# Optimization experiments

Hardware: AMD Instinct MI355X
Metric: run time of the kernel (lower is better)

Reference implementation:

```python
import jax, jax.numpy as jnp
import numpy as np

B, T, C = 4, 2048, 1024
QH = 4            # n_q_heads
D = C // QH       # per-head dim = 256
EPS = 1e-5


def setup_inputs() -> dict:
    key = jax.random.key(0)
    k1, k2, k3 = jax.random.split(key, 3)
    residual = jax.random.normal(k1, (B, T, C), dtype=jnp.float32)
    # scale weights ~ Xavier-ish so relu(score)^2 stays numerically sane
    w_fc = jax.random.normal(k2, (C, C), dtype=jnp.float32) * (1.0 / np.sqrt(C))
    w_proj = jax.random.normal(k3, (C, C), dtype=jnp.float32) * (1.0 / np.sqrt(C))
    ln_g = jnp.ones((C,), dtype=jnp.float32)
    ln_b = jnp.zeros((C,), dtype=jnp.float32)
    return {"residual": residual, "w_fc": w_fc, "w_proj": w_proj,
            "ln_g": ln_g, "ln_b": ln_b}


def _layernorm(x, g, b):
    mu = jnp.mean(x, axis=-1, keepdims=True)
    var = jnp.mean(jnp.square(x - mu), axis=-1, keepdims=True)
    return (x - mu) * jax.lax.rsqrt(var + EPS) * g + b


def reference(residual, w_fc, w_proj, ln_g, ln_b):
    Bx, Tx, Cx = residual.shape
    x = _layernorm(residual, ln_g, ln_b)
    # q: (B, QH, T, D)
    q = x.reshape(Bx, Tx, QH, D).transpose(0, 2, 1, 3)
    # keys: rows of w_fc chopped into 4C kv entries of dim D, shared across heads
    k = w_fc.reshape(-1, D)          # (S, D), S = 4C
    # values: columns of w_proj (i.e. w_proj^T rows) chopped the same way
    v = w_proj.T.reshape(-1, D)      # (S, D)
    scores = jnp.einsum('bhtd,sd->bhts', q, k)
    # softmax(log(relusq(score))) then *exp(lse) == plain relu(score)^2 weights
    p = jnp.square(jax.nn.relu(scores))
    out = jnp.einsum('bhts,sd->bhtd', p, v)
    out = out.transpose(0, 2, 1, 3).reshape(Bx, Tx, Cx)
    return residual + out
```

## Files before the change

### kernel.cpp

```cpp
#include <hip/hip_runtime.h>
#include <hip/hip_bf16.h>

typedef __attribute__((ext_vector_type(8))) short bf16x8;
typedef __attribute__((ext_vector_type(4))) float f32x4;

#define C_    1024
#define MROWS 32768
#define D_    256
#define S_TOT 4096
#define SCH   64
#define NCH   (S_TOT / SCH)

__device__ __forceinline__ unsigned short f2bf(float f) {
  union { float f; unsigned int u; } v; v.f = f;
  unsigned int u = v.u;
  u += 0x7fffu + ((u >> 16) & 1u);
  return (unsigned short)(u >> 16);
}

__device__ __forceinline__ void async16(const void* g, void* l) {
  __builtin_amdgcn_global_load_lds(
      (const __attribute__((address_space(1))) unsigned int*)g,
      (__attribute__((address_space(3))) unsigned int*)l, 16, 0, 0);
}

__global__ __launch_bounds__(256) void prep_all(
    const float* __restrict__ res, const float* __restrict__ g,
    const float* __restrict__ b, const float* __restrict__ wfc,
    const float* __restrict__ wproj,
    unsigned short* __restrict__ xq, unsigned short* __restrict__ kq,
    unsigned short* __restrict__ vq) {
  __shared__ unsigned short tile[8192];
  int bid = blockIdx.x;
  int tid = threadIdx.x;

  if (bid < 2048) {
    int wave = tid >> 6, lane = tid & 63;
    int row = bid * 4 + wave;
    const float* r = res + (size_t)row * C_;
    float4 x[4];
    float s = 0.f, s2 = 0.f;
    #pragma unroll
    for (int i = 0; i < 4; ++i) {
      x[i] = *(const float4*)(r + i * 256 + lane * 4);
      s  += x[i].x + x[i].y + x[i].z + x[i].w;
      s2 += x[i].x * x[i].x + x[i].y * x[i].y + x[i].z * x[i].z + x[i].w * x[i].w;
    }
    #pragma unroll
    for (int off = 32; off > 0; off >>= 1) {
      s  += __shfl_xor(s, off, 64);
      s2 += __shfl_xor(s2, off, 64);
    }
    float mu  = s * (1.0f / C_);
    float var = s2 * (1.0f / C_) - mu * mu;
    float rs  = rsqrtf(var + 1e-5f);
    #pragma unroll
    for (int i = 0; i < 4; ++i) {
      int c = i * 256 + lane * 4;
      float4 gg = *(const float4*)(g + c);
      float4 bb = *(const float4*)(b + c);
      unsigned short o[4];
      o[0] = f2bf((x[i].x - mu) * rs * gg.x + bb.x);
      o[1] = f2bf((x[i].y - mu) * rs * gg.y + bb.y);
      o[2] = f2bf((x[i].z - mu) * rs * gg.z + bb.z);
      o[3] = f2bf((x[i].w - mu) * rs * gg.w + bb.w);
      *(ushort4*)(xq + (size_t)row * C_ + c) = *(ushort4*)o;
    }
  } else if (bid < 2560) {
    int t = (bid - 2048) * 256 + tid;
    int lane = t & 63;
    int sn  = (t >> 6) & 1;
    int kc  = (t >> 7) & 7;
    int sc2 = t >> 10;
    int s = sc2 * 32 + sn * 16 + (lane & 15);
    int d = kc * 32 + (lane >> 4) * 8;
    const float* src = wfc + (size_t)s * D_ + d;
    float4 a = *(const float4*)src;
    float4 b2 = *(const float4*)(src + 4);
    unsigned short o[8] = { f2bf(a.x), f2bf(a.y), f2bf(a.z), f2bf(a.w),
                            f2bf(b2.x), f2bf(b2.y), f2bf(b2.z), f2bf(b2.w) };
    *(uint4*)(kq + (size_t)t * 8) = *(uint4*)o;
  } else {
    int bb = bid - 2560;
    int c0 = bb * 8;
    #pragma unroll
    for (int it = 0; it < 4; ++it) {
      int row = it * 256 + tid;
      const float* src = wproj + (size_t)row * C_ + c0;
      float4 a = *(const float4*)src;
      float4 b2 = *(const float4*)(src + 4);
      unsigned short* dst = &tile[row * 8];
      dst[0] = f2bf(a.x);  dst[1] = f2bf(a.y);  dst[2] = f2bf(a.z);  dst[3] = f2bf(a.w);
      dst[4] = f2bf(b2.x); dst[5] = f2bf(b2.y); dst[6] = f2bf(b2.z); dst[7] = f2bf(b2.w);
    }
    __syncthreads();
    #pragma unroll
    for (int it = 0; it < 4; ++it) {
      int slot = it * 256 + tid;
      int lane = slot & 63;
      int dn   = slot >> 6;
      int d = dn * 16 + (lane & 15);
      int sl0 = (lane >> 4) * 8;
      unsigned short o[8];
      #pragma unroll
      for (int j = 0; j < 8; ++j) {
        int sl = sl0 + j;
        o[j] = tile[((sl & 3) * 256 + d) * 8 + (sl >> 2)];
      }
      *(uint4*)(vq + (size_t)bb * 8192 + (size_t)slot * 8) = *(uint4*)o;
    }
  }
}

__global__ __launch_bounds__(512, 1) void mlpmha_main(
    const unsigned short* __restrict__ xq,
    const unsigned short* __restrict__ kq,
    const unsigned short* __restrict__ vq,
    const float* __restrict__ res,
    float* __restrict__ out) {
  __shared__ unsigned short ldsK[2][16384];
  __shared__ unsigned short ldsV[16384];
  __shared__ unsigned short ldsP[2][128][36];

  int tid  = threadIdx.x;
  int wave = tid >> 6;
  int lane = tid & 63;
  int l16  = lane & 15;
  int quad = lane >> 4;
  int wgM  = blockIdx.x * 128;

  int mi = wave & 1, si = wave >> 1;
  int sh = si >> 1, sl = si & 1;
  int ni = wave & 3, mi2 = wave >> 2;

  bf16x8 qf[4][8];
  #pragma unroll
  for (int mt = 0; mt < 4; ++mt) {
    const unsigned short* qr =
        xq + (size_t)(wgM + mi * 64 + mt * 16 + l16) * D_ + quad * 8;
    #pragma unroll
    for (int kc = 0; kc < 8; ++kc) qf[mt][kc] = *(const bf16x8*)(qr + kc * 32);
  }

  f32x4 acc[4][4];
  #pragma unroll
  for (int i = 0; i < 4; ++i)
    #pragma unroll
    for (int j = 0; j < 4; ++j) acc[i][j] = (f32x4){0.f, 0.f, 0.f, 0.f};

  int soff = tid * 8;

  {
    const unsigned short* kg = kq + soff;
    #pragma unroll
    for (int i = 0; i < 4; ++i)
      async16(kg + i * 4096, &ldsK[0][soff + i * 4096]);
  }
  __syncthreads();

  for (int sc = 0; sc < NCH; ++sc) {
    int cur = sc & 1;

    {
      const unsigned short* vg = vq + (size_t)sc * 16384 + soff;
      #pragma unroll
      for (int i = 0; i < 4; ++i)
        async16(vg + i * 4096, &ldsV[soff + i * 4096]);
    }

    f32x4 sacc[4];
    #pragma unroll
    for (int mt = 0; mt < 4; ++mt) sacc[mt] = (f32x4){0.f, 0.f, 0.f, 0.f};
    #pragma unroll
    for (int kc = 0; kc < 8; ++kc) {
      bf16x8 kb = *(const bf16x8*)&ldsK[cur][sh * 8192 + (kc * 2 + sl) * 512 + lane * 8];
      #pragma unroll
      for (int mt = 0; mt < 4; ++mt)
        sacc[mt] = __builtin_amdgcn_mfma_f32_16x16x32_bf16(qf[mt][kc], kb, sacc[mt], 0, 0, 0);
    }

    #pragma unroll
    for (int mt = 0; mt < 4; ++mt)
      #pragma unroll
      for (int r = 0; r < 4; ++r) {
        float v = sacc[mt][r];
        v = v > 0.f ? v * v : 0.f;
        ldsP[sh][mi * 64 + mt * 16 + quad * 4 + r][sl * 16 + l16] = f2bf(v);
      }

    __syncthreads();

    if (sc + 1 < NCH) {
      const unsigned short* kg = kq + (size_t)(sc + 1) * 16384 + soff;
      #pragma unroll
      for (int i = 0; i < 4; ++i)
        async16(kg + i * 4096, &ldsK[1 - cur][soff + i * 4096]);
    }

    #pragma unroll
    for (int h = 0; h < 2; ++h) {
      bf16x8 vb[4];
      #pragma unroll
      for (int dnl = 0; dnl < 4; ++dnl)
        vb[dnl] = *(const bf16x8*)&ldsV[h * 8192 + ((ni * 4 + dnl) * 64 + lane) * 8];
      #pragma unroll
      for (int mt2 = 0; mt2 < 4; ++mt2) {
        const unsigned short* pp = &ldsP[h][mi2 * 64 + mt2 * 16 + l16][quad * 8];
        union { ushort4 u4[2]; bf16x8 v; } pu;
        pu.u4[0] = *(const ushort4*)pp;
        pu.u4[1] = *(const ushort4*)(pp + 4);
        bf16x8 pa = pu.v;
        #pragma unroll
        for (int dnl = 0; dnl < 4; ++dnl)
          acc[mt2][dnl] = __builtin_amdgcn_mfma_f32_16x16x32_bf16(pa, vb[dnl], acc[mt2][dnl], 0, 0, 0);
      }
    }

    __syncthreads();
  }

  #pragma unroll
  for (int mt2 = 0; mt2 < 4; ++mt2)
    #pragma unroll
    for (int r = 0; r < 4; ++r) {
      size_t row = (size_t)(wgM + mi2 * 64 + mt2 * 16 + quad * 4 + r) * D_;
      #pragma unroll
      for (int dnl = 0; dnl < 4; ++dnl) {
        size_t idx = row + ni * 64 + dnl * 16 + l16;
        out[idx] = res[idx] + acc[mt2][dnl][r];
      }
    }
}

extern "C" void kernel_launch(void* const* d_in, const int* in_sizes, int n_in,
                              void* d_out, int out_size, void* d_ws, size_t ws_size,
                              hipStream_t stream) {
  const float* res   = (const float*)d_in[0];
  const float* wfc   = (const float*)d_in[1];
  const float* wproj = (const float*)d_in[2];
  const float* g     = (const float*)d_in[3];
  const float* b     = (const float*)d_in[4];
  float* out = (float*)d_out;

  unsigned short* xq = (unsigned short*)d_ws;
  unsigned short* kq = xq + (size_t)MROWS * D_;
  unsigned short* vq = kq + (size_t)S_TOT * D_;

  prep_all<<<2688, 256, 0, stream>>>(res, g, b, wfc, wproj, xq, kq, vq);
  mlpmha_main<<<256, 512, 0, stream>>>(xq, kq, vq, res, out);
}
```

Measured before the change: 259.0 us.

## Halve kv chunk, load K straight into registers, triple-buffer V, drop second barrier

```diff
diff --git a/kernel.cpp b/kernel.cpp
--- a/kernel.cpp
+++ b/kernel.cpp
@@ -8,7 +8,7 @@
 #define MROWS 32768
 #define D_    256
 #define S_TOT 4096
-#define SCH   64
+#define SCH   32
 #define NCH   (S_TOT / SCH)
 
 __device__ __forceinline__ unsigned short f2bf(float f) {
@@ -118,8 +118,7 @@
     const unsigned short* __restrict__ vq,
     const float* __restrict__ res,
     float* __restrict__ out) {
-  __shared__ unsigned short ldsK[2][16384];
-  __shared__ unsigned short ldsV[16384];
+  __shared__ unsigned short ldsV[3][8192];
   __shared__ unsigned short ldsP[2][128][36];
 
   int tid  = threadIdx.x;
@@ -129,15 +128,24 @@
   int quad = lane >> 4;
   int wgM  = blockIdx.x * 128;
 
-  int mi = wave & 1, si = wave >> 1;
-  int sh = si >> 1, sl = si & 1;
+  int mi = wave & 3, si = wave >> 2;
   int ni = wave & 3, mi2 = wave >> 2;
 
-  bf16x8 qf[4][8];
-  #pragma unroll
-  for (int mt = 0; mt < 4; ++mt) {
+  int soff = tid * 8;
+
+  {
+    const unsigned short* vg = vq + soff;
+    async16(vg, &ldsV[0][soff]);
+    async16(vg + 4096, &ldsV[0][soff + 4096]);
+    async16(vg + 8192, &ldsV[1][soff]);
+    async16(vg + 12288, &ldsV[1][soff + 4096]);
+  }
+
+  bf16x8 qf[2][8];
+  #pragma unroll
+  for (int mt = 0; mt < 2; ++mt) {
     const unsigned short* qr =
-        xq + (size_t)(wgM + mi * 64 + mt * 16 + l16) * D_ + quad * 8;
+        xq + (size_t)(wgM + mi * 32 + mt * 16 + l16) * D_ + quad * 8;
     #pragma unroll
     for (int kc = 0; kc < 8; ++kc) qf[mt][kc] = *(const bf16x8*)(qr + kc * 32);
   }
@@ -148,64 +156,59 @@
     #pragma unroll
     for (int j = 0; j < 4; ++j) acc[i][j] = (f32x4){0.f, 0.f, 0.f, 0.f};
 
-  int soff = tid * 8;
-
-  {
-    const unsigned short* kg = kq + soff;
-    #pragma unroll
-    for (int i = 0; i < 4; ++i)
-      async16(kg + i * 4096, &ldsK[0][soff + i * 4096]);
-  }
-  __syncthreads();
-
+  const unsigned short* kbase = kq + si * 512 + lane * 8;
+  bf16x8 kb[2][8];
+  #pragma unroll
+  for (int kc = 0; kc < 8; ++kc)
+    kb[0][kc] = *(const bf16x8*)(kbase + kc * 1024);
+
+  #pragma unroll 2
   for (int sc = 0; sc < NCH; ++sc) {
-    int cur = sc & 1;
-
-    {
-      const unsigned short* vg = vq + (size_t)sc * 16384 + soff;
-      #pragma unroll
-      for (int i = 0; i < 4; ++i)
-        async16(vg + i * 4096, &ldsV[soff + i * 4096]);
-    }
-
-    f32x4 sacc[4];
-    #pragma unroll
-    for (int mt = 0; mt < 4; ++mt) sacc[mt] = (f32x4){0.f, 0.f, 0.f, 0.f};
+    int kcur = sc & 1;
+    int pb   = sc & 1;
+    int vbuf = sc % 3;
+
+    f32x4 sacc[2];
+    sacc[0] = (f32x4){0.f, 0.f, 0.f, 0.f};
+    sacc[1] = (f32x4){0.f, 0.f, 0.f, 0.f};
     #pragma unroll
     for (int kc = 0; kc < 8; ++kc) {
-      bf16x8 kb = *(const bf16x8*)&ldsK[cur][sh * 8192 + (kc * 2 + sl) * 512 + lane * 8];
-      #pragma unroll
-      for (int mt = 0; mt < 4; ++mt)
-        sacc[mt] = __builtin_amdgcn_mfma_f32_16x16x32_bf16(qf[mt][kc], kb, sacc[mt], 0, 0, 0);
-    }
-
-    #pragma unroll
-    for (int mt = 0; mt < 4; ++mt)
+      #pragma unroll
+      for (int mt = 0; mt < 2; ++mt)
+        sacc[mt] = __builtin_amdgcn_mfma_f32_16x16x32_bf16(qf[mt][kc], kb[kcur][kc], sacc[mt], 0, 0, 0);
+    }
+
+    #pragma unroll
+    for (int mt = 0; mt < 2; ++mt)
       #pragma unroll
       for (int r = 0; r < 4; ++r) {
         float v = sacc[mt][r];
         v = v > 0.f ? v * v : 0.f;
-        ldsP[sh][mi * 64 + mt * 16 + quad * 4 + r][sl * 16 + l16] = f2bf(v);
+        ldsP[pb][mi * 32 + mt * 16 + quad * 4 + r][si * 16 + l16] = f2bf(v);
       }
 
     __syncthreads();
 
+    if (sc + 2 < NCH) {
+      const unsigned short* vg = vq + (size_t)(sc + 2) * 8192 + soff;
+      async16(vg, &ldsV[(sc + 2) % 3][soff]);
+      async16(vg + 4096, &ldsV[(sc + 2) % 3][soff + 4096]);
+    }
     if (sc + 1 < NCH) {
-      const unsigned short* kg = kq + (size_t)(sc + 1) * 16384 + soff;
-      #pragma unroll
-      for (int i = 0; i < 4; ++i)
-        async16(kg + i * 4096, &ldsK[1 - cur][soff + i * 4096]);
-    }
-
-    #pragma unroll
-    for (int h = 0; h < 2; ++h) {
+      const unsigned short* kn = kbase + (size_t)(sc + 1) * 8192;
+      #pragma unroll
+      for (int kc = 0; kc < 8; ++kc)
+        kb[1 - kcur][kc] = *(const bf16x8*)(kn + kc * 1024);
+    }
+
+    {
       bf16x8 vb[4];
       #pragma unroll
       for (int dnl = 0; dnl < 4; ++dnl)
-        vb[dnl] = *(const bf16x8*)&ldsV[h * 8192 + ((ni * 4 + dnl) * 64 + lane) * 8];
+        vb[dnl] = *(const bf16x8*)&ldsV[vbuf][((ni * 4 + dnl) * 64 + lane) * 8];
       #pragma unroll
       for (int mt2 = 0; mt2 < 4; ++mt2) {
-        const unsigned short* pp = &ldsP[h][mi2 * 64 + mt2 * 16 + l16][quad * 8];
+        const unsigned short* pp = &ldsP[pb][mi2 * 64 + mt2 * 16 + l16][quad * 8];
         union { ushort4 u4[2]; bf16x8 v; } pu;
         pu.u4[0] = *(const ushort4*)pp;
         pu.u4[1] = *(const ushort4*)(pp + 4);
@@ -215,8 +218,6 @@
           acc[mt2][dnl] = __builtin_amdgcn_mfma_f32_16x16x32_bf16(pa, vb[dnl], acc[mt2][dnl], 0, 0, 0);
       }
     }
-
-    __syncthreads();
   }
 
   #pragma unroll
```

Result: slower. 303.4 us (+17.1%).
